# Performance work log

Hardware: AMD Instinct MI355X
Metric: run time of the kernel (lower is better)

The kernel has to match this reference:

```python
import jax, jax.numpy as jnp
import numpy as np

B, S, E, H = 4, 2048, 2048, 1  # batch, seq, n_embd, n_head (source only runs with H=1)
LN_EPS = 1e-5


def _layernorm(x, g, b):
    m = jnp.mean(x, axis=-1, keepdims=True)
    v = jnp.mean(jnp.square(x - m), axis=-1, keepdims=True)
    return (x - m) * jax.lax.rsqrt(v + LN_EPS) * g + b


def setup_inputs() -> dict:
    key = jax.random.key(0)
    ks = jax.random.split(key, 8)
    sc = 0.02
    return {
        "x": jax.random.normal(ks[0], (B, S, E), jnp.float32),
        "mask": jnp.ones((B, S, 1, 1), jnp.int32),
        # attention params (torch Linear stored transposed: (in, out))
        "w_attn": jax.random.normal(ks[1], (E, H * E), jnp.float32) * sc,
        "b_attn": jnp.zeros((H * E,), jnp.float32),
        "w_kv": jax.random.normal(ks[2], (E, H * E), jnp.float32) * sc,
        "b_kv": jnp.zeros((H * E,), jnp.float32),
        "ln1_g": jnp.ones((E,), jnp.float32),
        "ln1_b": jnp.zeros((E,), jnp.float32),
        # MLP params
        "w_fc": jax.random.normal(ks[3], (E, 4 * E), jnp.float32) * sc,
        "b_fc": jnp.zeros((4 * E,), jnp.float32),
        "w_mproj": jax.random.normal(ks[4], (4 * E, E), jnp.float32) * sc,
        "b_mproj": jnp.zeros((E,), jnp.float32),
        "ln2_g": jnp.ones((E,), jnp.float32),
        "ln2_b": jnp.zeros((E,), jnp.float32),
    }


def reference(x, mask, w_attn, b_attn, w_kv, b_kv, ln1_g, ln1_b,
              w_fc, b_fc, w_mproj, b_mproj, ln2_g, ln2_b):
    # ---- Attention (faithful to source: einsum binds 'h' to the seq axis) ----
    h_attn = (x @ w_attn + b_attn).reshape(B, S, H, E)  # (b, s, h, d)
    h_proj = (x @ w_kv + b_kv).reshape(B, S, H, E)      # (b, s, h, d)
    # score[b, s, m, l] = sum_d h_attn[b, s, l, d] * h_proj[b, s, m, d]
    attn_score = jnp.einsum('bhld,bhmd->bhml', h_attn, h_proj)  # (B, S, H, H)
    attn_score = jnp.where(mask == 0, jnp.float32(-1e9), attn_score)
    attn_prob = jax.nn.softmax(attn_score, axis=-1)
    attn_vec = jnp.einsum('bhml,bhmd->bhld', attn_prob, h_proj)  # (B, S, H, E)
    attn_out = attn_vec.reshape(B, S, H * E)
    # (dropouts are identity in eval mode)
    # ---- Residual + LN + MLP + Residual + LN ----
    h = _layernorm(x + attn_out, ln1_g, ln1_b)
    h_mlp = jax.nn.gelu(h @ w_fc + b_fc, approximate=False)
    h_mlp = h_mlp @ w_mproj + b_mproj
    return _layernorm(h_mlp + x, ln2_g, ln2_b)
```

## Files before the change

### kernel.cpp

```cpp
#include <hip/hip_runtime.h>
#include <hip/hip_bf16.h>
#include <stdint.h>


typedef __attribute__((ext_vector_type(4))) float f32x4;
typedef __attribute__((ext_vector_type(8))) __bf16 bf16x8;
typedef __attribute__((ext_vector_type(8))) unsigned short ushort8;

__device__ __forceinline__ unsigned short f2bf(float f) {
  unsigned int u = __float_as_uint(f);
  return (unsigned short)((u + 0x7FFFu + ((u >> 16) & 1u)) >> 16);
}

__device__ __forceinline__ void gload_lds16(const void* g, void* l) {
  __builtin_amdgcn_global_load_lds(
      (const __attribute__((address_space(1))) unsigned int*)(uintptr_t)g,
      (__attribute__((address_space(3))) unsigned int*)(unsigned int)(uintptr_t)l,
      16, 0, 0);
}

__global__ __launch_bounds__(256) void cvt_bf16_kernel(
    const float* __restrict__ in, unsigned short* __restrict__ out, int n8) {
  int i = blockIdx.x * 256 + threadIdx.x;
  if (i >= n8) return;
  const size_t base = (size_t)i * 8;
  float4 a = *(const float4*)(in + base);
  float4 b = *(const float4*)(in + base + 4);
  ushort8 o;
  o[0] = f2bf(a.x); o[1] = f2bf(a.y); o[2] = f2bf(a.z); o[3] = f2bf(a.w);
  o[4] = f2bf(b.x); o[5] = f2bf(b.y); o[6] = f2bf(b.z); o[7] = f2bf(b.w);
  *(ushort8*)(out + base) = o;
}

__global__ __launch_bounds__(256) void transpose_cvt(
    const float* __restrict__ W, unsigned short* __restrict__ WT, int R, int C) {
  __shared__ unsigned short t[64][66];
  const int c0 = blockIdx.x * 64, r0 = blockIdx.y * 64;
  const int tid = threadIdx.x;
  const int lr = tid >> 4;
  const int lc = (tid & 15) * 4;
#pragma unroll
  for (int p = 0; p < 4; ++p) {
    const int r = lr + p * 16;
    float4 v = *(const float4*)(W + (size_t)(r0 + r) * C + c0 + lc);
    t[r][lc + 0] = f2bf(v.x);
    t[r][lc + 1] = f2bf(v.y);
    t[r][lc + 2] = f2bf(v.z);
    t[r][lc + 3] = f2bf(v.w);
  }
  __syncthreads();
#pragma unroll
  for (int p = 0; p < 4; ++p) {
    const int oc = lr + p * 16;
    ushort4 o;
    o.x = t[lc + 0][oc];
    o.y = t[lc + 1][oc];
    o.z = t[lc + 2][oc];
    o.w = t[lc + 3][oc];
    *(ushort4*)(WT + (size_t)(c0 + oc) * R + r0 + lc) = o;
  }
}

#define BM 128
#define BN 128
#define BK 64

template <int EPI>
__global__ __launch_bounds__(256, 3) void gemm_bf16(
    const unsigned short* __restrict__ A,
    const unsigned short* __restrict__ BT,
    const float* __restrict__ bias,
    const float* __restrict__ xres,
    void* __restrict__ out, int N, int K) {
  __shared__ alignas(16) unsigned short smA[BM * BK];
  __shared__ alignas(16) unsigned short smB[BN * BK];

  const int tid = threadIdx.x;
  const int lane = tid & 63;
  const int w = tid >> 6;
  const int wr = w >> 1, wc = w & 1;

  const int nbn = N / BN;
  const int nwg = gridDim.x;
  const int bid = blockIdx.x;
  const int wg = (bid & 7) * (nwg >> 3) + (bid >> 3);
  const int bm = wg / nbn, bn = wg % nbn;

  const int srow = (w << 5) + (lane >> 3);
  const int sc = (lane & 7) ^ ((lane >> 3) & 7);
  const unsigned short* gA = A + (size_t)(bm * BM + srow) * K + sc * 8;
  const unsigned short* gB = BT + (size_t)(bn * BN + srow) * K + sc * 8;
  unsigned short* lA = smA + (w << 5) * BK;
  unsigned short* lB = smB + (w << 5) * BK;

  const int arow = (wr << 6) + (lane & 15);
  const int brow = (wc << 6) + (lane & 15);
  const int kg = lane >> 4;
  const int r7 = lane & 7;

  f32x4 acc[4][4] = {};

  const int nkt = K / BK;
  for (int kt = 0; kt < nkt; ++kt) {
    const size_t koff = (size_t)kt * BK;
#pragma unroll
    for (int i = 0; i < 4; ++i) {
      gload_lds16(gA + (size_t)(i * 8) * K + koff, lA + i * 8 * BK);
      gload_lds16(gB + (size_t)(i * 8) * K + koff, lB + i * 8 * BK);
    }
    __syncthreads();
#pragma unroll
    for (int kk = 0; kk < 2; ++kk) {
      bf16x8 af[4], bfr[4];
#pragma unroll
      for (int m = 0; m < 4; ++m) {
        const int off = (arow + m * 16) * (BK * 2) + ((((kk << 2) + kg) ^ r7) << 4);
        af[m] = *reinterpret_cast<const bf16x8*>((const char*)smA + off);
      }
#pragma unroll
      for (int n = 0; n < 4; ++n) {
        const int off = (brow + n * 16) * (BK * 2) + ((((kk << 2) + kg) ^ r7) << 4);
        bfr[n] = *reinterpret_cast<const bf16x8*>((const char*)smB + off);
      }
#pragma unroll
      for (int m = 0; m < 4; ++m)
#pragma unroll
        for (int n = 0; n < 4; ++n)
          acc[m][n] = __builtin_amdgcn_mfma_f32_16x16x32_bf16(
              af[m], bfr[n], acc[m][n], 0, 0, 0);
    }
    __syncthreads();
  }

  const int col0 = bn * BN + (wc << 6) + (lane & 15);
  const int row0 = bm * BM + (wr << 6) + ((lane >> 4) << 2);
  float bv[4];
#pragma unroll
  for (int n = 0; n < 4; ++n) bv[n] = bias[col0 + n * 16];
#pragma unroll
  for (int m = 0; m < 4; ++m) {
#pragma unroll
    for (int j = 0; j < 4; ++j) {
      const size_t row = (size_t)(row0 + m * 16 + j);
#pragma unroll
      for (int n = 0; n < 4; ++n) {
        const size_t idx = row * N + col0 + n * 16;
        float v = acc[m][n][j] + bv[n];
        if (EPI == 0) {
          ((float*)out)[idx] = v + xres[idx];
        } else {
          float ge = 0.5f * v * (1.0f + erff(v * 0.7071067811865475f));
          ((unsigned short*)out)[idx] = f2bf(ge);
        }
      }
    }
  }
}

template <int OUT_BF16>
__global__ __launch_bounds__(256) void ln_row(const float* __restrict__ tin,
                                              const float* __restrict__ gw,
                                              const float* __restrict__ bw,
                                              void* __restrict__ outp) {
  const int row = blockIdx.x;
  const int tid = threadIdx.x;
  const size_t base = (size_t)row * 2048 + tid * 8;
  alignas(16) float v[8];
  *(float4*)(v) = *(const float4*)(tin + base);
  *(float4*)(v + 4) = *(const float4*)(tin + base + 4);
  float s = 0.f, q = 0.f;
#pragma unroll
  for (int i = 0; i < 8; ++i) { s += v[i]; q += v[i] * v[i]; }
#pragma unroll
  for (int m = 32; m >= 1; m >>= 1) {
    s += __shfl_xor(s, m);
    q += __shfl_xor(q, m);
  }
  __shared__ float red[8];
  if ((tid & 63) == 0) {
    red[tid >> 6] = s;
    red[4 + (tid >> 6)] = q;
  }
  __syncthreads();
  s = red[0] + red[1] + red[2] + red[3];
  q = red[4] + red[5] + red[6] + red[7];
  const float mean = s * (1.0f / 2048.0f);
  float var = q * (1.0f / 2048.0f) - mean * mean;
  var = fmaxf(var, 0.0f);
  const float rstd = rsqrtf(var + 1e-5f);
  alignas(16) float gv[8], bv[8];
  *(float4*)(gv) = *(const float4*)(gw + (size_t)tid * 8);
  *(float4*)(gv + 4) = *(const float4*)(gw + (size_t)tid * 8 + 4);
  *(float4*)(bv) = *(const float4*)(bw + (size_t)tid * 8);
  *(float4*)(bv + 4) = *(const float4*)(bw + (size_t)tid * 8 + 4);
  if (OUT_BF16) {
    ushort8 o;
#pragma unroll
    for (int i = 0; i < 8; ++i)
      o[i] = f2bf((v[i] - mean) * rstd * gv[i] + bv[i]);
    *(ushort8*)((unsigned short*)outp + base) = o;
  } else {
    alignas(16) float r[8];
#pragma unroll
    for (int i = 0; i < 8; ++i) r[i] = (v[i] - mean) * rstd * gv[i] + bv[i];
    *(float4*)((float*)outp + base) = *(float4*)(r);
    *(float4*)((float*)outp + base + 4) = *(float4*)(r + 4);
  }
}

extern "C" void kernel_launch(void* const* d_in, const int* in_sizes, int n_in,
                              void* d_out, int out_size, void* d_ws,
                              size_t ws_size, hipStream_t stream) {
  constexpr int M = 8192;
  constexpr int E = 2048;
  constexpr int F = 8192;
  const size_t MiB = 1ull << 20;

  const float* x = (const float*)d_in[0];
  const float* w_kv = (const float*)d_in[4];
  const float* b_kv = (const float*)d_in[5];
  const float* ln1_g = (const float*)d_in[6];
  const float* ln1_b = (const float*)d_in[7];
  const float* w_fc = (const float*)d_in[8];
  const float* b_fc = (const float*)d_in[9];
  const float* w_mproj = (const float*)d_in[10];
  const float* b_mproj = (const float*)d_in[11];
  const float* ln2_g = (const float*)d_in[12];
  const float* ln2_b = (const float*)d_in[13];
  float* out = (float*)d_out;
  char* ws = (char*)d_ws;

  float* tbuf = out;

  int nch;
  unsigned short *xb, *wkvT, *wfcT, *wmpT, *hb, *gch;
  if (ws_size >= 224 * MiB) {
    nch = 1;
    gch = (unsigned short*)(ws + 0);
    xb = (unsigned short*)(ws + 0);
    wkvT = (unsigned short*)(ws + 32 * MiB);
    wfcT = (unsigned short*)(ws + 128 * MiB);
    wmpT = (unsigned short*)(ws + 160 * MiB);
    hb = (unsigned short*)(ws + 192 * MiB);
  } else {
    nch = 4;
    xb = (unsigned short*)(ws + 0);
    gch = (unsigned short*)(ws + 0);
    wkvT = (unsigned short*)(ws + 32 * MiB);
    hb = (unsigned short*)(ws + 32 * MiB);
    wfcT = (unsigned short*)(ws + 64 * MiB);
    wmpT = (unsigned short*)(ws + 96 * MiB);
  }

  cvt_bf16_kernel<<<(M * E / 8 + 255) / 256, 256, 0, stream>>>(x, xb, M * E / 8);
  transpose_cvt<<<dim3(E / 64, E / 64), 256, 0, stream>>>(w_kv, wkvT, E, E);
  transpose_cvt<<<dim3(F / 64, E / 64), 256, 0, stream>>>(w_fc, wfcT, E, F);
  transpose_cvt<<<dim3(E / 64, F / 64), 256, 0, stream>>>(w_mproj, wmpT, F, E);
  gemm_bf16<0><<<(M / BM) * (E / BN), 256, 0, stream>>>(xb, wkvT, b_kv, x, tbuf,
                                                        E, E);
  ln_row<1><<<M, 256, 0, stream>>>(tbuf, ln1_g, ln1_b, hb);
  const int Mc = M / nch;
  for (int c = 0; c < nch; ++c) {
    const size_t roff = (size_t)c * Mc;
    gemm_bf16<1><<<(Mc / BM) * (F / BN), 256, 0, stream>>>(
        hb + roff * E, wfcT, b_fc, nullptr, gch, F, E);
    gemm_bf16<0><<<(Mc / BM) * (E / BN), 256, 0, stream>>>(
        gch, wmpT, b_mproj, x + roff * E, tbuf + roff * E, E, F);
  }
  ln_row<0><<<M, 256, 0, stream>>>(tbuf, ln2_g, ln2_b, out);
}
```

Baseline: 805.1 us.

## Replace 128x128 GEMM with 256x256 double-buffered 8-wave pipelined GEMM

Swaps the single-buffered 128x128 tile GEMM for a 256x256-tile, 512-thread kernel. It double-buffers LDS and interleaves global-to-LDS loads of the next tiles with MFMA on the current one, using barriers, waitcnt and setprio to schedule the phases. Larger tiles raise arithmetic intensity and cut global traffic, and the pipeline hides load latency. It also adds a 2-chunk workspace layout for mid-sized workspaces. The cost is 128KB of LDS per block and fewer workgroups, which may hurt occupancy or tail balance on small chunked grids.

```diff
diff --git a/kernel.cpp b/kernel.cpp
--- a/kernel.cpp
+++ b/kernel.cpp
@@ -61,91 +61,162 @@
   }
 }
 
-#define BM 128
-#define BN 128
-#define BK 64
-
 template <int EPI>
-__global__ __launch_bounds__(256, 3) void gemm_bf16(
-    const unsigned short* __restrict__ A,
-    const unsigned short* __restrict__ BT,
-    const float* __restrict__ bias,
-    const float* __restrict__ xres,
+__global__ __launch_bounds__(512, 2) void gemm256(
+    const unsigned short* __restrict__ A, const unsigned short* __restrict__ BT,
+    const float* __restrict__ bias, const float* __restrict__ xres,
     void* __restrict__ out, int N, int K) {
-  __shared__ alignas(16) unsigned short smA[BM * BK];
-  __shared__ alignas(16) unsigned short smB[BN * BK];
+  __shared__ unsigned short lds[2][2][256 * 64];
 
   const int tid = threadIdx.x;
   const int lane = tid & 63;
   const int w = tid >> 6;
-  const int wr = w >> 1, wc = w & 1;
-
-  const int nbn = N / BN;
+  const int wm = w >> 2;
+  const int wn = w & 3;
+
+  const int nbn = N / 256;
   const int nwg = gridDim.x;
   const int bid = blockIdx.x;
   const int wg = (bid & 7) * (nwg >> 3) + (bid >> 3);
   const int bm = wg / nbn, bn = wg % nbn;
 
-  const int srow = (w << 5) + (lane >> 3);
-  const int sc = (lane & 7) ^ ((lane >> 3) & 7);
-  const unsigned short* gA = A + (size_t)(bm * BM + srow) * K + sc * 8;
-  const unsigned short* gB = BT + (size_t)(bn * BN + srow) * K + sc * 8;
-  unsigned short* lA = smA + (w << 5) * BK;
-  unsigned short* lB = smB + (w << 5) * BK;
-
-  const int arow = (wr << 6) + (lane & 15);
-  const int brow = (wc << 6) + (lane & 15);
-  const int kg = lane >> 4;
-  const int r7 = lane & 7;
-
-  f32x4 acc[4][4] = {};
-
-  const int nkt = K / BK;
-  for (int kt = 0; kt < nkt; ++kt) {
-    const size_t koff = (size_t)kt * BK;
-#pragma unroll
-    for (int i = 0; i < 4; ++i) {
-      gload_lds16(gA + (size_t)(i * 8) * K + koff, lA + i * 8 * BK);
-      gload_lds16(gB + (size_t)(i * 8) * K + koff, lB + i * 8 * BK);
-    }
-    __syncthreads();
-#pragma unroll
-    for (int kk = 0; kk < 2; ++kk) {
-      bf16x8 af[4], bfr[4];
-#pragma unroll
-      for (int m = 0; m < 4; ++m) {
-        const int off = (arow + m * 16) * (BK * 2) + ((((kk << 2) + kg) ^ r7) << 4);
-        af[m] = *reinterpret_cast<const bf16x8*>((const char*)smA + off);
-      }
-#pragma unroll
-      for (int n = 0; n < 4; ++n) {
-        const int off = (brow + n * 16) * (BK * 2) + ((((kk << 2) + kg) ^ r7) << 4);
-        bfr[n] = *reinterpret_cast<const bf16x8*>((const char*)smB + off);
-      }
-#pragma unroll
-      for (int m = 0; m < 4; ++m)
-#pragma unroll
-        for (int n = 0; n < 4; ++n)
-          acc[m][n] = __builtin_amdgcn_mfma_f32_16x16x32_bf16(
-              af[m], bfr[n], acc[m][n], 0, 0, 0);
-    }
-    __syncthreads();
-  }
-
-  const int col0 = bn * BN + (wc << 6) + (lane & 15);
-  const int row0 = bm * BM + (wr << 6) + ((lane >> 4) << 2);
+  const int nt = K / 64;
+
+  const int srow = w * 8 + (lane >> 3);
+  const int schunk = (lane & 7) ^ ((lane >> 3) & 7);
+  const unsigned short* gA = A + (size_t)(bm * 256 + srow) * K + schunk * 8;
+  const unsigned short* gB = BT + (size_t)(bn * 256 + srow) * K + schunk * 8;
+
+  auto STAGE = [&](int buf, int op, int half, int tile) {
+    const int tc = tile < nt ? tile : nt - 1;
+    const unsigned short* g =
+        (op ? gB : gA) + (size_t)(half * 128) * K + (size_t)tc * 64;
+    unsigned short* l = &lds[buf][op][(half * 128 + w * 8) * 64];
+    gload_lds16(g, l);
+    gload_lds16(g + (size_t)64 * K, l + 64 * 64);
+  };
+
+  const int rA = wm * 128 + (lane & 15);
+  const int rB = wn * 64 + (lane & 15);
+  const int kq = lane >> 4;
+  const int x7 = lane & 7;
+
+  auto LDA = [&](int buf, int mh, int mf, int ks) -> bf16x8 {
+    const char* p = (const char*)&lds[buf][0][0] +
+                    (rA + mh * 64 + mf * 16) * 128 +
+                    (((ks * 4 + kq) ^ x7) << 4);
+    return *(const bf16x8*)p;
+  };
+  auto LDB = [&](int buf, int nh, int nf, int ks) -> bf16x8 {
+    const char* p = (const char*)&lds[buf][1][0] +
+                    (rB + nh * 32 + nf * 16) * 128 +
+                    (((ks * 4 + kq) ^ x7) << 4);
+    return *(const bf16x8*)p;
+  };
+
+  f32x4 acc[8][4] = {};
+  bf16x8 aLo[4][2], aHi[4][2], bfr[2][2];
+
+  STAGE(0, 0, 0, 0); STAGE(0, 0, 1, 0); STAGE(0, 1, 0, 0); STAGE(0, 1, 1, 0);
+  STAGE(1, 0, 0, 1); STAGE(1, 0, 1, 1); STAGE(1, 1, 0, 1);
+  asm volatile("s_waitcnt vmcnt(6)" ::: "memory");
+  __builtin_amdgcn_s_barrier();
+
+  for (int t = 0; t < nt; ++t) {
+    const int cb = t & 1, ob = cb ^ 1;
+#pragma unroll
+    for (int mf = 0; mf < 4; ++mf)
+#pragma unroll
+      for (int ks = 0; ks < 2; ++ks) aLo[mf][ks] = LDA(cb, 0, mf, ks);
+#pragma unroll
+    for (int nf = 0; nf < 2; ++nf)
+#pragma unroll
+      for (int ks = 0; ks < 2; ++ks) bfr[nf][ks] = LDB(cb, 0, nf, ks);
+    STAGE(ob, 1, 1, t + 1);
+    __builtin_amdgcn_s_barrier();
+    asm volatile("s_waitcnt lgkmcnt(0)" ::: "memory");
+    __builtin_amdgcn_sched_barrier(0);
+    __builtin_amdgcn_s_setprio(1);
+#pragma unroll
+    for (int mf = 0; mf < 4; ++mf)
+#pragma unroll
+      for (int nf = 0; nf < 2; ++nf)
+#pragma unroll
+        for (int ks = 0; ks < 2; ++ks)
+          acc[mf][nf] = __builtin_amdgcn_mfma_f32_16x16x32_bf16(
+              aLo[mf][ks], bfr[nf][ks], acc[mf][nf], 0, 0, 0);
+    __builtin_amdgcn_s_setprio(0);
+    __builtin_amdgcn_s_barrier();
+#pragma unroll
+    for (int mf = 0; mf < 4; ++mf)
+#pragma unroll
+      for (int ks = 0; ks < 2; ++ks) aHi[mf][ks] = LDA(cb, 1, mf, ks);
+    __builtin_amdgcn_s_barrier();
+    asm volatile("s_waitcnt lgkmcnt(0)" ::: "memory");
+    __builtin_amdgcn_sched_barrier(0);
+    __builtin_amdgcn_s_setprio(1);
+#pragma unroll
+    for (int mf = 0; mf < 4; ++mf)
+#pragma unroll
+      for (int nf = 0; nf < 2; ++nf)
+#pragma unroll
+        for (int ks = 0; ks < 2; ++ks)
+          acc[4 + mf][nf] = __builtin_amdgcn_mfma_f32_16x16x32_bf16(
+              aHi[mf][ks], bfr[nf][ks], acc[4 + mf][nf], 0, 0, 0);
+    __builtin_amdgcn_s_setprio(0);
+    __builtin_amdgcn_s_barrier();
+#pragma unroll
+    for (int nf = 0; nf < 2; ++nf)
+#pragma unroll
+      for (int ks = 0; ks < 2; ++ks) bfr[nf][ks] = LDB(cb, 1, nf, ks);
+    STAGE(cb, 0, 0, t + 2);
+    __builtin_amdgcn_s_barrier();
+    asm volatile("s_waitcnt lgkmcnt(0)" ::: "memory");
+    __builtin_amdgcn_sched_barrier(0);
+    __builtin_amdgcn_s_setprio(1);
+#pragma unroll
+    for (int mf = 0; mf < 4; ++mf)
+#pragma unroll
+      for (int nf = 0; nf < 2; ++nf)
+#pragma unroll
+        for (int ks = 0; ks < 2; ++ks)
+          acc[4 + mf][2 + nf] = __builtin_amdgcn_mfma_f32_16x16x32_bf16(
+              aHi[mf][ks], bfr[nf][ks], acc[4 + mf][2 + nf], 0, 0, 0);
+    __builtin_amdgcn_s_setprio(0);
+    __builtin_amdgcn_s_barrier();
+    STAGE(cb, 0, 1, t + 2);
+    STAGE(cb, 1, 0, t + 2);
+    __builtin_amdgcn_s_barrier();
+    __builtin_amdgcn_sched_barrier(0);
+    __builtin_amdgcn_s_setprio(1);
+#pragma unroll
+    for (int mf = 0; mf < 4; ++mf)
+#pragma unroll
+      for (int nf = 0; nf < 2; ++nf)
+#pragma unroll
+        for (int ks = 0; ks < 2; ++ks)
+          acc[mf][2 + nf] = __builtin_amdgcn_mfma_f32_16x16x32_bf16(
+              aLo[mf][ks], bfr[nf][ks], acc[mf][2 + nf], 0, 0, 0);
+    __builtin_amdgcn_s_setprio(0);
+    asm volatile("s_waitcnt vmcnt(6)" ::: "memory");
+    __builtin_amdgcn_s_barrier();
+  }
+  asm volatile("s_waitcnt vmcnt(0)" ::: "memory");
+
+  const int col0 = bn * 256 + wn * 64 + (lane & 15);
+  const int row0 = bm * 256 + wm * 128 + ((lane >> 4) << 2);
   float bv[4];
 #pragma unroll
   for (int n = 0; n < 4; ++n) bv[n] = bias[col0 + n * 16];
 #pragma unroll
-  for (int m = 0; m < 4; ++m) {
+  for (int mf = 0; mf < 8; ++mf) {
 #pragma unroll
     for (int j = 0; j < 4; ++j) {
-      const size_t row = (size_t)(row0 + m * 16 + j);
+      const size_t row = (size_t)(row0 + mf * 16 + j);
 #pragma unroll
       for (int n = 0; n < 4; ++n) {
         const size_t idx = row * N + col0 + n * 16;
-        float v = acc[m][n][j] + bv[n];
+        float v = acc[mf][n][j] + bv[n];
         if (EPI == 0) {
           ((float*)out)[idx] = v + xres[idx];
         } else {
@@ -242,10 +313,18 @@
     wfcT = (unsigned short*)(ws + 128 * MiB);
     wmpT = (unsigned short*)(ws + 160 * MiB);
     hb = (unsigned short*)(ws + 192 * MiB);
+  } else if (ws_size >= 160 * MiB) {
+    nch = 2;
+    gch = (unsigned short*)(ws + 0);
+    xb = (unsigned short*)(ws + 0);
+    wkvT = (unsigned short*)(ws + 32 * MiB);
+    hb = (unsigned short*)(ws + 64 * MiB);
+    wfcT = (unsigned short*)(ws + 96 * MiB);
+    wmpT = (unsigned short*)(ws + 128 * MiB);
   } else {
     nch = 4;
+    gch = (unsigned short*)(ws + 0);
     xb = (unsigned short*)(ws + 0);
-    gch = (unsigned short*)(ws + 0);
     wkvT = (unsigned short*)(ws + 32 * MiB);
     hb = (unsigned short*)(ws + 32 * MiB);
     wfcT = (unsigned short*)(ws + 64 * MiB);
@@ -256,15 +335,16 @@
   transpose_cvt<<<dim3(E / 64, E / 64), 256, 0, stream>>>(w_kv, wkvT, E, E);
   transpose_cvt<<<dim3(F / 64, E / 64), 256, 0, stream>>>(w_fc, wfcT, E, F);
   transpose_cvt<<<dim3(E / 64, F / 64), 256, 0, stream>>>(w_mproj, wmpT, F, E);
-  gemm_bf16<0><<<(M / BM) * (E / BN), 256, 0, stream>>>(xb, wkvT, b_kv, x, tbuf,
-                                                        E, E);
+
+  gemm256<0><<<(M / 256) * (E / 256), 512, 0, stream>>>(xb, wkvT, b_kv, x,
+                                                        tbuf, E, E);
   ln_row<1><<<M, 256, 0, stream>>>(tbuf, ln1_g, ln1_b, hb);
   const int Mc = M / nch;
   for (int c = 0; c < nch; ++c) {
     const size_t roff = (size_t)c * Mc;
-    gemm_bf16<1><<<(Mc / BM) * (F / BN), 256, 0, stream>>>(
+    gemm256<1><<<(Mc / 256) * (F / 256), 512, 0, stream>>>(
         hb + roff * E, wfcT, b_fc, nullptr, gch, F, E);
-    gemm_bf16<0><<<(Mc / BM) * (E / BN), 256, 0, stream>>>(
+    gemm256<0><<<(Mc / 256) * (E / 256), 512, 0, stream>>>(
         gch, wmpT, b_mproj, x + roff * E, tbuf + roff * E, E, F);
   }
   ln_row<0><<<M, 256, 0, stream>>>(tbuf, ln2_g, ln2_b, out);
```

Result: faster. 706.3 us (-12.3%).
